# Performance work log

Measured on AMD Instinct MI355X. Metric: run time of the kernel, lower is better.

## Reference

```python
import jax, jax.numpy as jnp
import numpy as np

DIMS = 1024
STATE = 2 * DIMS
EPS = 1e-8


def _rmsnorm(v, scale):
    # norm = ||v||_2 * d^{-1/2}
    d = v.shape[-1]
    n = jnp.sqrt(jnp.sum(v * v, axis=-1, keepdims=True)) * (d ** -0.5)
    return scale * v / (n + EPS)


def setup_inputs() -> dict:
    key = jax.random.key(0)
    ks = jax.random.split(key, 5)
    x = jax.random.normal(ks[0], (4, 2048, DIMS), dtype=jnp.float32)
    ls_scale = jnp.ones((DIMS // 2,), dtype=jnp.float32)
    rs_scale = jnp.ones((DIMS // 2,), dtype=jnp.float32)
    split_scale = jnp.full((DIMS,), 0.1, dtype=jnp.float32)
    sk = (1.0 / DIMS) ** 0.5
    Wk = jax.random.uniform(ks[1], (DIMS, STATE), jnp.float32, -sk, sk)
    Wugg = jax.random.uniform(ks[2], (DIMS, 3 * STATE), jnp.float32, -sk, sk)
    so = (1.0 / STATE) ** 0.5
    Wout = jax.random.uniform(ks[3], (STATE, DIMS), jnp.float32, -so, so)
    return {"x": x, "ls_scale": ls_scale, "rs_scale": rs_scale,
            "split_scale": split_scale, "Wk": Wk, "Wugg": Wugg, "Wout": Wout}


def reference(x, ls_scale, rs_scale, split_scale, Wk, Wugg, Wout):
    residual = x
    # RMS_split norm (output_dim=None)
    xl, xr = jnp.split(x, 2, axis=-1)
    xn = jnp.concatenate([_rmsnorm(xl, ls_scale), _rmsnorm(xr, rs_scale)], axis=-1)
    xn = xn * split_scale

    K = jax.nn.sigmoid(xn @ Wk)                      # [B,S,STATE]
    u, g_in, g_out = jnp.split(xn @ Wugg, 3, axis=-1)
    u = u * jax.nn.sigmoid(g_in) * (1.0 - K)

    # linear recurrence: h_0 = u_0; h_t = K_{t-1} * h_{t-1} + u_t
    a = jnp.concatenate([jnp.ones_like(K[..., :1, :]), K[..., :-1, :]], axis=-2)

    def combine(lhs, rhs):
        aL, bL = lhs
        aR, bR = rhs
        return (aL * aR, bL * aR + bR)

    _, h = jax.lax.associative_scan(combine, (a, u), axis=1)
    outputs = h * jax.nn.sigmoid(g_out)
    y = outputs @ Wout
    return y + residual
```

## Files before the change

### kernel.cpp

```cpp
#include <hip/hip_runtime.h>
#include <hip/hip_bf16.h>
#include <stdint.h>

#define DIMS 1024
#define STATE 2048
#define BATCH 4
#define SEQ 2048
#define TOKENS 8192
#define N1 8192
#define NCHUNK 16
#define CHUNKL (SEQ / NCHUNK)

typedef __hip_bfloat16 bf16;
typedef __attribute__((ext_vector_type(8))) short bf16x8;
typedef __attribute__((ext_vector_type(4))) float f32x4;
typedef __attribute__((ext_vector_type(16))) float f32x16;

__device__ __forceinline__ float sigmoidf_(float x) {
  return 1.0f / (1.0f + __expf(-x));
}

__device__ __forceinline__ void async_copy16(const void* g, void* l) {
  __builtin_amdgcn_global_load_lds(
      (const __attribute__((address_space(1))) void*)(uintptr_t)g,
      (__attribute__((address_space(3))) void*)(uint32_t)(uintptr_t)l,
      16, 0, 0);
}

__device__ __forceinline__ int swz64(int row, int kc) {
  return (row << 3) | (kc ^ (row & 7));
}
__device__ __forceinline__ void swz64_dec(int c, int& row, int& kc) {
  row = c >> 3;
  kc = (c & 7) ^ (row & 7);
}

__global__ __launch_bounds__(256) void transpose_bf16_kernel(
    const float* __restrict__ W, bf16* __restrict__ Wt, int K, int N) {
  __shared__ float tile[32][33];
  int tx = threadIdx.x & 31;
  int ty = threadIdx.x >> 5;
  long col = (long)blockIdx.x * 32 + tx;
  long rowb = (long)blockIdx.y * 32;
#pragma unroll
  for (int i = 0; i < 32; i += 8)
    tile[ty + i][tx] = W[(rowb + ty + i) * N + col];
  __syncthreads();
  long ocol = rowb + tx;
  long orow = (long)blockIdx.x * 32 + ty;
#pragma unroll
  for (int i = 0; i < 32; i += 8)
    Wt[(orow + i) * K + ocol] = __float2bfloat16(tile[tx][ty + i]);
}

__global__ __launch_bounds__(256) void rmsnorm_kernel(
    const float* __restrict__ x, const float* __restrict__ ls,
    const float* __restrict__ rs, const float* __restrict__ ss,
    bf16* __restrict__ xn) {
  int token = blockIdx.x;
  int tid = threadIdx.x;
  const float4* xt = (const float4*)(x + (long)token * DIMS);
  float4 v = xt[tid];
  float s = v.x * v.x + v.y * v.y + v.z * v.z + v.w * v.w;
#pragma unroll
  for (int d = 32; d > 0; d >>= 1) s += __shfl_down(s, d);
  __shared__ float parts[4];
  if ((tid & 63) == 0) parts[tid >> 6] = s;
  __syncthreads();
  int j = tid * 4;
  bool left = j < 512;
  float sum = left ? (parts[0] + parts[1]) : (parts[2] + parts[3]);
  float n = sqrtf(sum * (1.0f / 512.0f));
  float inv = 1.0f / (n + 1e-8f);
  const float4* sc = (const float4*)(left ? ls : rs);
  float4 g = sc[left ? tid : tid - 128];
  float4 p = ((const float4*)ss)[tid];
  bf16* o = xn + (long)token * DIMS + j;
  o[0] = __float2bfloat16(v.x * g.x * inv * p.x);
  o[1] = __float2bfloat16(v.y * g.y * inv * p.y);
  o[2] = __float2bfloat16(v.z * g.z * inv * p.z);
  o[3] = __float2bfloat16(v.w * g.w * inv * p.w);
}

__global__ __launch_bounds__(256, 2) void gemm1_big(
    const bf16* __restrict__ A, const bf16* __restrict__ Bt, bf16* __restrict__ C) {
  __shared__ __align__(16) bf16 As[256 * 64];
  __shared__ __align__(16) bf16 Bs[128 * 64];
  const int K = DIMS;
  int tid = threadIdx.x;
  int lane = tid & 63, wave = tid >> 6;
  int wm = wave & 1, wn = wave >> 1;
  long arow0 = (long)blockIdx.y * 256;
  long brow0 = (long)blockIdx.x * 128;
  int m_lane = lane & 31, q4 = lane >> 5;
  f32x16 acc[4][2] = {};

  for (int k0 = 0; k0 < K; k0 += 64) {
    __syncthreads();
#pragma unroll
    for (int i = 0; i < 8; i++) {
      int c = (wave * 8 + i) * 64 + lane;
      int row, kc; swz64_dec(c, row, kc);
      async_copy16(A + (arow0 + row) * K + k0 + kc * 8, (char*)As + (wave * 8 + i) * 1024);
    }
#pragma unroll
    for (int i = 0; i < 4; i++) {
      int c = (wave * 4 + i) * 64 + lane;
      int row, kc; swz64_dec(c, row, kc);
      async_copy16(Bt + (brow0 + row) * K + k0 + kc * 8, (char*)Bs + (wave * 4 + i) * 1024);
    }
    __syncthreads();
    const bf16x8* AsV = (const bf16x8*)As;
    const bf16x8* BsV = (const bf16x8*)Bs;
#pragma unroll
    for (int ks = 0; ks < 4; ks++) {
      int kc = ks * 2 + q4;
      bf16x8 af[4], bfr[2];
#pragma unroll
      for (int mt = 0; mt < 4; mt++)
        af[mt] = AsV[swz64(wm * 128 + mt * 32 + m_lane, kc)];
#pragma unroll
      for (int nt = 0; nt < 2; nt++)
        bfr[nt] = BsV[swz64(wn * 64 + nt * 32 + m_lane, kc)];
#pragma unroll
      for (int mt = 0; mt < 4; mt++)
#pragma unroll
        for (int nt = 0; nt < 2; nt++)
          acc[mt][nt] = __builtin_amdgcn_mfma_f32_32x32x16_bf16(bfr[nt], af[mt], acc[mt][nt], 0, 0, 0);
    }
  }
#pragma unroll
  for (int mt = 0; mt < 4; mt++) {
    long row = arow0 + wm * 128 + mt * 32 + m_lane;
#pragma unroll
    for (int nt = 0; nt < 2; nt++) {
#pragma unroll
      for (int g = 0; g < 4; g++) {
        long col = brow0 + wn * 64 + nt * 32 + g * 8 + q4 * 4;
        bf16 tmp[4];
#pragma unroll
        for (int j = 0; j < 4; j++) tmp[j] = __float2bfloat16(acc[mt][nt][g * 4 + j]);
        *(uint2*)(C + row * N1 + col) = *(uint2*)tmp;
      }
    }
  }
}

template <int EPI>
__global__ __launch_bounds__(256) void gemm_bt(
    const bf16* __restrict__ A, const bf16* __restrict__ Bt,
    void* __restrict__ Cout, const float* __restrict__ resid,
    int M, int N, int K) {
  __shared__ __align__(16) bf16 As[128 * 64];
  __shared__ __align__(16) bf16 Bs[128 * 64];
  int tid = threadIdx.x;
  int lane = tid & 63, wave = tid >> 6;
  int wm = wave & 1, wn = wave >> 1;
  long arow0 = (long)blockIdx.y * 128;
  long brow0 = (long)blockIdx.x * 128;
  int r = lane & 15, q = lane >> 4;
  f32x4 acc[4][4] = {};

  for (int k0 = 0; k0 < K; k0 += 64) {
    __syncthreads();
#pragma unroll
    for (int i = 0; i < 4; i++) {
      int c = (wave * 4 + i) * 64 + lane;
      int row, kc; swz64_dec(c, row, kc);
      async_copy16(A + (arow0 + row) * K + k0 + kc * 8, (char*)As + (wave * 4 + i) * 1024);
      async_copy16(Bt + (brow0 + row) * K + k0 + kc * 8, (char*)Bs + (wave * 4 + i) * 1024);
    }
    __syncthreads();
    const bf16x8* AsV = (const bf16x8*)As;
    const bf16x8* BsV = (const bf16x8*)Bs;
#pragma unroll
    for (int ks = 0; ks < 2; ks++) {
      bf16x8 af[4], bfr[4];
#pragma unroll
      for (int mt = 0; mt < 4; mt++) af[mt] = AsV[swz64(wm * 64 + mt * 16 + r, ks * 4 + q)];
#pragma unroll
      for (int nt = 0; nt < 4; nt++) bfr[nt] = BsV[swz64(wn * 64 + nt * 16 + r, ks * 4 + q)];
#pragma unroll
      for (int mt = 0; mt < 4; mt++)
#pragma unroll
        for (int nt = 0; nt < 4; nt++)
          acc[mt][nt] = __builtin_amdgcn_mfma_f32_16x16x32_bf16(bfr[nt], af[mt], acc[mt][nt], 0, 0, 0);
    }
  }

  if (EPI == 0) {
    bf16* C = (bf16*)Cout;
#pragma unroll
    for (int mt = 0; mt < 4; mt++) {
      long row = arow0 + wm * 64 + mt * 16 + r;
#pragma unroll
      for (int nt = 0; nt < 4; nt++) {
        long col = brow0 + wn * 64 + nt * 16 + q * 4;
        bf16 tmp[4];
#pragma unroll
        for (int reg = 0; reg < 4; reg++) tmp[reg] = __float2bfloat16(acc[mt][nt][reg]);
        *(uint2*)(C + row * N + col) = *(uint2*)tmp;
      }
    }
  } else {
    float* C = (float*)Cout;
#pragma unroll
    for (int mt = 0; mt < 4; mt++) {
      long row = arow0 + wm * 64 + mt * 16 + r;
#pragma unroll
      for (int nt = 0; nt < 4; nt++) {
        long col = brow0 + wn * 64 + nt * 16 + q * 4;
        float4 rv = *(const float4*)(resid + row * N + col);
        float4 ov;
        ov.x = acc[mt][nt][0] + rv.x;
        ov.y = acc[mt][nt][1] + rv.y;
        ov.z = acc[mt][nt][2] + rv.z;
        ov.w = acc[mt][nt][3] + rv.w;
        *(float4*)(C + row * N + col) = ov;
      }
    }
  }
}


__global__ __launch_bounds__(256) void chunk_summary_kernel(
    const bf16* __restrict__ C1, float* __restrict__ carryA,
    float* __restrict__ carryU) {
  int b = blockIdx.x;
  int ch = blockIdx.y * 256 + threadIdx.x;
  int chunk = blockIdx.z;
  int t0 = chunk * CHUNKL;
  long base = ((long)b * SEQ) * N1 + ch;
  float kp = 0.0f;
  if (chunk != 0) kp = __bfloat162float(C1[base + (long)(t0 - 1) * N1]);
  float a_first = (chunk == 0) ? 1.0f : sigmoidf_(kp);
  float A = 1.0f, U = 0.0f;
#pragma unroll 8
  for (int t = t0; t < t0 + CHUNKL; t++) {
    long off = base + (long)t * N1;
    float kraw = __bfloat162float(C1[off]);
    float uraw = __bfloat162float(C1[off + 2048]);
    float gin  = __bfloat162float(C1[off + 4096]);
    float a = (t == t0) ? a_first : sigmoidf_(kp);
    float sK = sigmoidf_(kraw);
    float u = uraw * sigmoidf_(gin) * (1.0f - sK);
    A *= a;
    U = a * U + u;
    kp = kraw;
  }
  int cidx = (b * NCHUNK + chunk) * STATE + ch;
  carryA[cidx] = A;
  carryU[cidx] = U;
}

__global__ __launch_bounds__(256) void carry_scan_kernel(
    const float* __restrict__ carryA, const float* __restrict__ carryU,
    float* __restrict__ carryIn) {
  int idx = blockIdx.x * 256 + threadIdx.x;
  int b = idx >> 11;
  int ch = idx & 2047;
  float h = 0.0f;
#pragma unroll
  for (int c = 0; c < NCHUNK; c++) {
    int cidx = (b * NCHUNK + c) * STATE + ch;
    carryIn[cidx] = h;
    h = carryA[cidx] * h + carryU[cidx];
  }
}

__global__ __launch_bounds__(256) void scan_chunk_kernel(
    const bf16* __restrict__ C1, const float* __restrict__ carryIn,
    bf16* __restrict__ out) {
  int b = blockIdx.x;
  int c0 = blockIdx.y * 32;
  int chunk = blockIdx.z;
  int tstart = chunk * CHUNKL;
  __shared__ float a_s[32][65], u_s[32][65], h_s[32][65];
  int tid = threadIdx.x;
  int lane = tid & 63, wave = tid >> 6;
  int cc = tid & 31;
  int tq = tid >> 5;

  float carryH[8], carryK[8];
#pragma unroll
  for (int i = 0; i < 8; i++) {
    int ch = c0 + wave * 8 + i;
    carryH[i] = carryIn[(b * NCHUNK + chunk) * STATE + ch];
    carryK[i] = (chunk == 0)
                    ? 1.0f
                    : sigmoidf_(__bfloat162float(
                          C1[((long)(b * SEQ + tstart - 1)) * N1 + ch]));
  }

  float g_r[8];
  for (int t0 = tstart; t0 < tstart + CHUNKL; t0 += 64) {
#pragma unroll
    for (int i = 0; i < 8; i++) {
      int t = tq * 8 + i;
      long rowoff = ((long)(b * SEQ + t0 + t)) * N1 + c0 + cc;
      float kraw = __bfloat162float(C1[rowoff]);
      float uraw = __bfloat162float(C1[rowoff + 2048]);
      float gin  = __bfloat162float(C1[rowoff + 4096]);
      float gout = __bfloat162float(C1[rowoff + 6144]);
      float aK = sigmoidf_(kraw);
      a_s[cc][t] = aK;
      u_s[cc][t] = uraw * sigmoidf_(gin) * (1.0f - aK);
      g_r[i] = sigmoidf_(gout);
    }
    __syncthreads();
#pragma unroll
    for (int i = 0; i < 8; i++) {
      int ch = wave * 8 + i;
      float aK = a_s[ch][lane];
      float u = u_s[ch][lane];
      float a = __shfl_up(aK, 1);
      if (lane == 0) a = carryK[i];
      float A = a, U = u;
#pragma unroll
      for (int d = 1; d < 64; d <<= 1) {
        float Au = __shfl_up(A, d);
        float Uu = __shfl_up(U, d);
        if (lane >= d) { U += A * Uu; A *= Au; }
      }
      float h = U + A * carryH[i];
      carryH[i] = __shfl(h, 63);
      carryK[i] = __shfl(aK, 63);
      h_s[ch][lane] = h;
    }
    __syncthreads();
#pragma unroll
    for (int i = 0; i < 8; i++) {
      int t = tq * 8 + i;
      out[((long)(b * SEQ + t0 + t)) * STATE + c0 + cc] =
          __float2bfloat16(h_s[cc][t] * g_r[i]);
    }
    __syncthreads();
  }
}

extern "C" void kernel_launch(void* const* d_in, const int* in_sizes, int n_in,
                              void* d_out, int out_size, void* d_ws, size_t ws_size,
                              hipStream_t stream) {
  const float* x    = (const float*)d_in[0];
  const float* ls   = (const float*)d_in[1];
  const float* rs   = (const float*)d_in[2];
  const float* ss   = (const float*)d_in[3];
  const float* Wk   = (const float*)d_in[4];
  const float* Wugg = (const float*)d_in[5];
  const float* Wout = (const float*)d_in[6];
  float* out = (float*)d_out;

  char* ws = (char*)d_ws;
  bf16* W1t = (bf16*)ws;
  bf16* W2t = (bf16*)(ws + 16777216);
  bf16* xn  = (bf16*)(ws + 16777216 + 4194304);
  bf16* C1  = (bf16*)(ws + 16777216 + 4194304 + 16777216);
  bf16* sco = (bf16*)(ws + 16777216 + 4194304 + 16777216 + 134217728);
  float* carryA  = (float*)xn;
  float* carryU  = carryA + BATCH * NCHUNK * STATE;
  float* carryIn = carryU + BATCH * NCHUNK * STATE;

  transpose_bf16_kernel<<<dim3(STATE / 32, DIMS / 32), 256, 0, stream>>>(Wk, W1t, DIMS, STATE);
  transpose_bf16_kernel<<<dim3(3 * STATE / 32, DIMS / 32), 256, 0, stream>>>(
      Wugg, W1t + (long)STATE * DIMS, DIMS, 3 * STATE);
  transpose_bf16_kernel<<<dim3(DIMS / 32, STATE / 32), 256, 0, stream>>>(Wout, W2t, STATE, DIMS);

  rmsnorm_kernel<<<TOKENS, 256, 0, stream>>>(x, ls, rs, ss, xn);

  gemm1_big<<<dim3(N1 / 128, TOKENS / 256), 256, 0, stream>>>(xn, W1t, C1);

  chunk_summary_kernel<<<dim3(BATCH, STATE / 256, NCHUNK), 256, 0, stream>>>(
      C1, carryA, carryU);
  carry_scan_kernel<<<dim3(BATCH * STATE / 256), 256, 0, stream>>>(
      carryA, carryU, carryIn);
  scan_chunk_kernel<<<dim3(BATCH, STATE / 32, NCHUNK), 256, 0, stream>>>(
      C1, carryIn, sco);

  gemm_bt<1><<<dim3(DIMS / 128, TOKENS / 128), 256, 0, stream>>>(
      sco, W2t, (void*)out, x, TOKENS, DIMS, STATE);
}
```

Measured before the change: 445.6 us.

## Double-buffer LDS in both GEMMs to overlap global loads with MFMA

Both GEMMs move from a single-buffer load-sync-compute loop to ping-pong LDS buffers. The next K-slice is issued asynchronously while MFMAs run on the current one, which removes one barrier per step. gemm1 halves its K-step to 32 to keep the LDS footprint the same, using a new swizzle for 32-wide rows. gemm2 doubles its LDS to 64KB, which may limit occupancy. The generic gemm_bt template is specialized into a residual-epilogue kernel.

```diff
diff --git a/kernel.cpp b/kernel.cpp
--- a/kernel.cpp
+++ b/kernel.cpp
@@ -27,6 +27,17 @@
       16, 0, 0);
 }
 
+__device__ __forceinline__ int swz32(int row, int kc) {
+  int line = row >> 1;
+  int sub = ((row & 1) << 2) | kc;
+  return (line << 3) | (sub ^ (line & 7));
+}
+__device__ __forceinline__ void swz32_dec(int c, int& row, int& kc) {
+  int line = c >> 3;
+  int sub = (c & 7) ^ (line & 7);
+  row = (line << 1) | (sub >> 2);
+  kc = sub & 3;
+}
 __device__ __forceinline__ int swz64(int row, int kc) {
   return (row << 3) | (kc ^ (row & 7));
 }
@@ -82,11 +93,29 @@
   o[3] = __float2bfloat16(v.w * g.w * inv * p.w);
 }
 
+__device__ __forceinline__ void g1_stage(const bf16* __restrict__ A,
+                                         const bf16* __restrict__ Bt,
+                                         long arow0, long brow0, int k0,
+                                         int wave, int lane, bf16* As, bf16* Bs) {
+  const int K = DIMS;
+#pragma unroll
+  for (int i = 0; i < 4; i++) {
+    int c = (wave * 4 + i) * 64 + lane;
+    int row, kc; swz32_dec(c, row, kc);
+    async_copy16(A + (arow0 + row) * K + k0 + kc * 8, (char*)As + (wave * 4 + i) * 1024);
+  }
+#pragma unroll
+  for (int i = 0; i < 2; i++) {
+    int c = (wave * 2 + i) * 64 + lane;
+    int row, kc; swz32_dec(c, row, kc);
+    async_copy16(Bt + (brow0 + row) * K + k0 + kc * 8, (char*)Bs + (wave * 2 + i) * 1024);
+  }
+}
+
 __global__ __launch_bounds__(256, 2) void gemm1_big(
     const bf16* __restrict__ A, const bf16* __restrict__ Bt, bf16* __restrict__ C) {
-  __shared__ __align__(16) bf16 As[256 * 64];
-  __shared__ __align__(16) bf16 Bs[128 * 64];
-  const int K = DIMS;
+  __shared__ __align__(16) bf16 As0[256 * 32], As1[256 * 32];
+  __shared__ __align__(16) bf16 Bs0[128 * 32], Bs1[128 * 32];
   int tid = threadIdx.x;
   int lane = tid & 63, wave = tid >> 6;
   int wm = wave & 1, wn = wave >> 1;
@@ -95,38 +124,54 @@
   int m_lane = lane & 31, q4 = lane >> 5;
   f32x16 acc[4][2] = {};
 
-  for (int k0 = 0; k0 < K; k0 += 64) {
-    __syncthreads();
-#pragma unroll
-    for (int i = 0; i < 8; i++) {
-      int c = (wave * 8 + i) * 64 + lane;
-      int row, kc; swz64_dec(c, row, kc);
-      async_copy16(A + (arow0 + row) * K + k0 + kc * 8, (char*)As + (wave * 8 + i) * 1024);
-    }
-#pragma unroll
-    for (int i = 0; i < 4; i++) {
-      int c = (wave * 4 + i) * 64 + lane;
-      int row, kc; swz64_dec(c, row, kc);
-      async_copy16(Bt + (brow0 + row) * K + k0 + kc * 8, (char*)Bs + (wave * 4 + i) * 1024);
-    }
-    __syncthreads();
-    const bf16x8* AsV = (const bf16x8*)As;
-    const bf16x8* BsV = (const bf16x8*)Bs;
-#pragma unroll
-    for (int ks = 0; ks < 4; ks++) {
-      int kc = ks * 2 + q4;
-      bf16x8 af[4], bfr[2];
-#pragma unroll
-      for (int mt = 0; mt < 4; mt++)
-        af[mt] = AsV[swz64(wm * 128 + mt * 32 + m_lane, kc)];
-#pragma unroll
-      for (int nt = 0; nt < 2; nt++)
-        bfr[nt] = BsV[swz64(wn * 64 + nt * 32 + m_lane, kc)];
-#pragma unroll
-      for (int mt = 0; mt < 4; mt++)
-#pragma unroll
-        for (int nt = 0; nt < 2; nt++)
-          acc[mt][nt] = __builtin_amdgcn_mfma_f32_32x32x16_bf16(bfr[nt], af[mt], acc[mt][nt], 0, 0, 0);
+  g1_stage(A, Bt, arow0, brow0, 0, wave, lane, As0, Bs0);
+  __syncthreads();
+
+  for (int it = 0; it < 32; it += 2) {
+    {
+      const bf16x8* AsV = (const bf16x8*)As0;
+      const bf16x8* BsV = (const bf16x8*)Bs0;
+      bf16x8 af[2][4], bfr[2][2];
+#pragma unroll
+      for (int ks = 0; ks < 2; ks++) {
+        int kc = ks * 2 + q4;
+#pragma unroll
+        for (int mt = 0; mt < 4; mt++) af[ks][mt] = AsV[swz32(wm * 128 + mt * 32 + m_lane, kc)];
+#pragma unroll
+        for (int nt = 0; nt < 2; nt++) bfr[ks][nt] = BsV[swz32(wn * 64 + nt * 32 + m_lane, kc)];
+      }
+      g1_stage(A, Bt, arow0, brow0, (it + 1) * 32, wave, lane, As1, Bs1);
+#pragma unroll
+      for (int ks = 0; ks < 2; ks++)
+#pragma unroll
+        for (int mt = 0; mt < 4; mt++)
+#pragma unroll
+          for (int nt = 0; nt < 2; nt++)
+            acc[mt][nt] = __builtin_amdgcn_mfma_f32_32x32x16_bf16(bfr[ks][nt], af[ks][mt], acc[mt][nt], 0, 0, 0);
+      __syncthreads();
+    }
+    {
+      const bf16x8* AsV = (const bf16x8*)As1;
+      const bf16x8* BsV = (const bf16x8*)Bs1;
+      bf16x8 af[2][4], bfr[2][2];
+#pragma unroll
+      for (int ks = 0; ks < 2; ks++) {
+        int kc = ks * 2 + q4;
+#pragma unroll
+        for (int mt = 0; mt < 4; mt++) af[ks][mt] = AsV[swz32(wm * 128 + mt * 32 + m_lane, kc)];
+#pragma unroll
+        for (int nt = 0; nt < 2; nt++) bfr[ks][nt] = BsV[swz32(wn * 64 + nt * 32 + m_lane, kc)];
+      }
+      if (it + 2 < 32)
+        g1_stage(A, Bt, arow0, brow0, (it + 2) * 32, wave, lane, As0, Bs0);
+#pragma unroll
+      for (int ks = 0; ks < 2; ks++)
+#pragma unroll
+        for (int mt = 0; mt < 4; mt++)
+#pragma unroll
+          for (int nt = 0; nt < 2; nt++)
+            acc[mt][nt] = __builtin_amdgcn_mfma_f32_32x32x16_bf16(bfr[ks][nt], af[ks][mt], acc[mt][nt], 0, 0, 0);
+      __syncthreads();
     }
   }
 #pragma unroll
@@ -146,13 +191,25 @@
   }
 }
 
-template <int EPI>
-__global__ __launch_bounds__(256) void gemm_bt(
+__device__ __forceinline__ void g2_stage(const bf16* __restrict__ A,
+                                         const bf16* __restrict__ Bt,
+                                         long arow0, long brow0, int k0, int K,
+                                         int wave, int lane, bf16* As, bf16* Bs) {
+#pragma unroll
+  for (int i = 0; i < 4; i++) {
+    int c = (wave * 4 + i) * 64 + lane;
+    int row, kc; swz64_dec(c, row, kc);
+    async_copy16(A + (arow0 + row) * K + k0 + kc * 8, (char*)As + (wave * 4 + i) * 1024);
+    async_copy16(Bt + (brow0 + row) * K + k0 + kc * 8, (char*)Bs + (wave * 4 + i) * 1024);
+  }
+}
+
+__global__ __launch_bounds__(256) void gemm2_resid(
     const bf16* __restrict__ A, const bf16* __restrict__ Bt,
-    void* __restrict__ Cout, const float* __restrict__ resid,
-    int M, int N, int K) {
-  __shared__ __align__(16) bf16 As[128 * 64];
-  __shared__ __align__(16) bf16 Bs[128 * 64];
+    float* __restrict__ C, const float* __restrict__ resid) {
+  __shared__ __align__(16) bf16 As0[128 * 64], As1[128 * 64];
+  __shared__ __align__(16) bf16 Bs0[128 * 64], Bs1[128 * 64];
+  const int K = STATE, N = DIMS;
   int tid = threadIdx.x;
   int lane = tid & 63, wave = tid >> 6;
   int wm = wave & 1, wn = wave >> 1;
@@ -161,63 +218,68 @@
   int r = lane & 15, q = lane >> 4;
   f32x4 acc[4][4] = {};
 
-  for (int k0 = 0; k0 < K; k0 += 64) {
-    __syncthreads();
-#pragma unroll
-    for (int i = 0; i < 4; i++) {
-      int c = (wave * 4 + i) * 64 + lane;
-      int row, kc; swz64_dec(c, row, kc);
-      async_copy16(A + (arow0 + row) * K + k0 + kc * 8, (char*)As + (wave * 4 + i) * 1024);
-      async_copy16(Bt + (brow0 + row) * K + k0 + kc * 8, (char*)Bs + (wave * 4 + i) * 1024);
-    }
-    __syncthreads();
-    const bf16x8* AsV = (const bf16x8*)As;
-    const bf16x8* BsV = (const bf16x8*)Bs;
-#pragma unroll
-    for (int ks = 0; ks < 2; ks++) {
-      bf16x8 af[4], bfr[4];
-#pragma unroll
-      for (int mt = 0; mt < 4; mt++) af[mt] = AsV[swz64(wm * 64 + mt * 16 + r, ks * 4 + q)];
-#pragma unroll
-      for (int nt = 0; nt < 4; nt++) bfr[nt] = BsV[swz64(wn * 64 + nt * 16 + r, ks * 4 + q)];
-#pragma unroll
-      for (int mt = 0; mt < 4; mt++)
-#pragma unroll
-        for (int nt = 0; nt < 4; nt++)
-          acc[mt][nt] = __builtin_amdgcn_mfma_f32_16x16x32_bf16(bfr[nt], af[mt], acc[mt][nt], 0, 0, 0);
-    }
-  }
-
-  if (EPI == 0) {
-    bf16* C = (bf16*)Cout;
-#pragma unroll
-    for (int mt = 0; mt < 4; mt++) {
-      long row = arow0 + wm * 64 + mt * 16 + r;
-#pragma unroll
-      for (int nt = 0; nt < 4; nt++) {
-        long col = brow0 + wn * 64 + nt * 16 + q * 4;
-        bf16 tmp[4];
-#pragma unroll
-        for (int reg = 0; reg < 4; reg++) tmp[reg] = __float2bfloat16(acc[mt][nt][reg]);
-        *(uint2*)(C + row * N + col) = *(uint2*)tmp;
-      }
-    }
-  } else {
-    float* C = (float*)Cout;
-#pragma unroll
-    for (int mt = 0; mt < 4; mt++) {
-      long row = arow0 + wm * 64 + mt * 16 + r;
-#pragma unroll
-      for (int nt = 0; nt < 4; nt++) {
-        long col = brow0 + wn * 64 + nt * 16 + q * 4;
-        float4 rv = *(const float4*)(resid + row * N + col);
-        float4 ov;
-        ov.x = acc[mt][nt][0] + rv.x;
-        ov.y = acc[mt][nt][1] + rv.y;
-        ov.z = acc[mt][nt][2] + rv.z;
-        ov.w = acc[mt][nt][3] + rv.w;
-        *(float4*)(C + row * N + col) = ov;
-      }
+  g2_stage(A, Bt, arow0, brow0, 0, K, wave, lane, As0, Bs0);
+  __syncthreads();
+
+  for (int it = 0; it < 32; it += 2) {
+    {
+      const bf16x8* AsV = (const bf16x8*)As0;
+      const bf16x8* BsV = (const bf16x8*)Bs0;
+      bf16x8 af[2][4], bfr[2][4];
+#pragma unroll
+      for (int ks = 0; ks < 2; ks++) {
+#pragma unroll
+        for (int mt = 0; mt < 4; mt++) af[ks][mt] = AsV[swz64(wm * 64 + mt * 16 + r, ks * 4 + q)];
+#pragma unroll
+        for (int nt = 0; nt < 4; nt++) bfr[ks][nt] = BsV[swz64(wn * 64 + nt * 16 + r, ks * 4 + q)];
+      }
+      g2_stage(A, Bt, arow0, brow0, (it + 1) * 64, K, wave, lane, As1, Bs1);
+#pragma unroll
+      for (int ks = 0; ks < 2; ks++)
+#pragma unroll
+        for (int mt = 0; mt < 4; mt++)
+#pragma unroll
+          for (int nt = 0; nt < 4; nt++)
+            acc[mt][nt] = __builtin_amdgcn_mfma_f32_16x16x32_bf16(bfr[ks][nt], af[ks][mt], acc[mt][nt], 0, 0, 0);
+      __syncthreads();
+    }
+    {
+      const bf16x8* AsV = (const bf16x8*)As1;
+      const bf16x8* BsV = (const bf16x8*)Bs1;
+      bf16x8 af[2][4], bfr[2][4];
+#pragma unroll
+      for (int ks = 0; ks < 2; ks++) {
+#pragma unroll
+        for (int mt = 0; mt < 4; mt++) af[ks][mt] = AsV[swz64(wm * 64 + mt * 16 + r, ks * 4 + q)];
+#pragma unroll
+        for (int nt = 0; nt < 4; nt++) bfr[ks][nt] = BsV[swz64(wn * 64 + nt * 16 + r, ks * 4 + q)];
+      }
+      if (it + 2 < 32)
+        g2_stage(A, Bt, arow0, brow0, (it + 2) * 64, K, wave, lane, As0, Bs0);
+#pragma unroll
+      for (int ks = 0; ks < 2; ks++)
+#pragma unroll
+        for (int mt = 0; mt < 4; mt++)
+#pragma unroll
+          for (int nt = 0; nt < 4; nt++)
+            acc[mt][nt] = __builtin_amdgcn_mfma_f32_16x16x32_bf16(bfr[ks][nt], af[ks][mt], acc[mt][nt], 0, 0, 0);
+      __syncthreads();
+    }
+  }
+
+#pragma unroll
+  for (int mt = 0; mt < 4; mt++) {
+    long row = arow0 + wm * 64 + mt * 16 + r;
+#pragma unroll
+    for (int nt = 0; nt < 4; nt++) {
+      long col = brow0 + wn * 64 + nt * 16 + q * 4;
+      float4 rv = *(const float4*)(resid + row * N + col);
+      float4 ov;
+      ov.x = acc[mt][nt][0] + rv.x;
+      ov.y = acc[mt][nt][1] + rv.y;
+      ov.z = acc[mt][nt][2] + rv.z;
+      ov.w = acc[mt][nt][3] + rv.w;
+      *(float4*)(C + row * N + col) = ov;
     }
   }
 }
@@ -376,6 +438,6 @@
   scan_chunk_kernel<<<dim3(BATCH, STATE / 32, NCHUNK), 256, 0, stream>>>(
       C1, carryIn, sco);
 
-  gemm_bt<1><<<dim3(DIMS / 128, TOKENS / 128), 256, 0, stream>>>(
-      sco, W2t, (void*)out, x, TOKENS, DIMS, STATE);
-}
+  gemm2_resid<<<dim3(DIMS / 128, TOKENS / 128), 256, 0, stream>>>(
+      sco, W2t, out, x);
+}
```

New measurement: 444.8 us. About the same (-0.2%).
